# Kernel tuning notes

Hardware: AMD Instinct MI355X
Metric: run time of the kernel (lower is better)

The kernel has to match this reference:

```python
import jax, jax.numpy as jnp
import numpy as np

SMALL = 1e-16
N = 8192      # num_nodes
D_IN = 512    # input_dim
D_LAT = 128   # latent_dim


def setup_inputs() -> dict:
    key = jax.random.key(0)
    ks = jax.random.split(key, 6)
    z = jax.random.normal(ks[0], (N, D_IN), jnp.float32)
    gamma = jax.random.uniform(ks[1], (N, D_IN), jnp.float32)
    delta = jax.random.uniform(ks[2], (N, D_IN), jnp.float32)
    lim = float(np.sqrt(6.0 / (D_IN + D_LAT)))  # glorot-uniform init
    Wz = jax.random.uniform(ks[3], (D_IN, D_LAT), jnp.float32, -lim, lim)
    Wg = jax.random.uniform(ks[4], (D_IN, D_LAT), jnp.float32, -lim, lim)
    Wd = jax.random.uniform(ks[5], (D_IN, D_LAT), jnp.float32, -lim, lim)
    return {
        "z": z, "gamma": gamma, "delta": delta,
        "Wz": Wz, "Wg": Wg, "Wd": Wd,
        "bias": jnp.float32(1.0),
        "w_gam": jnp.float32(0.5),
        "w_del": jnp.float32(0.5),
    }


def reference(z, gamma, delta, Wz, Wg, Wd, bias, w_gam, w_del):
    # column-stochastic transforms (softmax over input_dim axis, as in __init__)
    Tz = jax.nn.softmax(Wz, axis=0)
    Tg = jax.nn.softmax(Wg, axis=0)
    Td = jax.nn.softmax(Wd, axis=0)

    zd = z @ Tz                 # [N, D_LAT]
    gd_raw = gamma @ Tg         # [N, D_LAT]
    dd_raw = delta @ Td         # [N, D_LAT]
    gd = gd_raw + SMALL
    dd = dd_raw + SMALL

    z2 = zd * zd
    # dist_gam[i,j] = sum_k (zd[i,k]-zd[j,k])^2 / gd[i,k]  (sender-scaled)
    # expanded: sum_k z2_i/g_i  +  (1/g_i) . z2_j  -  2 (z_i/g_i) . z_j
    a = jnp.sum(z2 / gd, axis=1)                                  # [N]
    dist_gam = a[:, None] + (1.0 / gd) @ z2.T - 2.0 * (zd / gd) @ zd.T  # [N,N]

    # dist_del[i,j] = sum_k (zd[i,k]-zd[j,k])^2 / dd[j,k]  (receiver-scaled)
    b = jnp.sum(z2 / dd, axis=1)                                  # [N]
    dist_del = z2 @ (1.0 / dd).T - 2.0 * zd @ (zd / dd).T + b[None, :]  # [N,N]

    n = jnp.float32(N)
    x = bias - w_gam * (n * dist_gam) - w_del * (n * dist_del)
    out = jax.nn.sigmoid(x.reshape(-1))                           # [N*N]
    return out, zd, gd_raw, dd_raw
```

## Files before the change

### kernel.cpp

```cpp
#include <hip/hip_runtime.h>
#include <hip/hip_bf16.h>
#include <math.h>


#define NSZ 8192
#define DLAT 128

typedef _Float16 half8 __attribute__((ext_vector_type(8)));
typedef float f32x4 __attribute__((ext_vector_type(4)));
typedef float f32x16 __attribute__((ext_vector_type(16)));

__device__ __forceinline__ void gl_lds16(const void* g, void* l) {
    __builtin_amdgcn_global_load_lds(
        (const __attribute__((address_space(1))) void*)g,
        (__attribute__((address_space(3))) void*)l, 16, 0, 0);
}

__device__ __forceinline__ float fast_sigmoid(float x) {
    float e = __builtin_amdgcn_exp2f(-1.44269504f * x);
    return __builtin_amdgcn_rcpf(1.0f + e);
}

__global__ void softmax_cols(const float* __restrict__ Wz, const float* __restrict__ Wg,
                             const float* __restrict__ Wd, _Float16* __restrict__ Tt) {
    int col = blockIdx.x & 127;
    int m = blockIdx.x >> 7;
    const float* W = (m == 0) ? Wz : (m == 1 ? Wg : Wd);
    _Float16* To = Tt + (size_t)m * 65536 + (size_t)col * 512;
    int l = threadIdx.x;
    float v[8];
    float mx = -3.4e38f;
    for (int i = 0; i < 8; ++i) {
        v[i] = W[(size_t)(i * 64 + l) * 128 + col];
        mx = fmaxf(mx, v[i]);
    }
    for (int off = 32; off; off >>= 1) mx = fmaxf(mx, __shfl_xor(mx, off));
    float s = 0.f;
    for (int i = 0; i < 8; ++i) { v[i] = expf(v[i] - mx); s += v[i]; }
    for (int off = 32; off; off >>= 1) s += __shfl_xor(s, off);
    float inv = 1.0f / s;
    for (int i = 0; i < 8; ++i) To[i * 64 + l] = (_Float16)(v[i] * inv);
}

__global__ __launch_bounds__(128) void gemm3_mfma(const float* __restrict__ z,
                                                  const float* __restrict__ gamma,
                                                  const float* __restrict__ delta,
                                                  const _Float16* __restrict__ Tt,
                                                  float* __restrict__ outTail) {
    int m = blockIdx.y;
    const float* A = (m == 0) ? z : (m == 1 ? gamma : delta);
    const _Float16* B = Tt + (size_t)m * 65536;
    float* C = outTail + (size_t)m * (NSZ * DLAT);
    int rowBase = blockIdx.x * 32;
    __shared__ _Float16 As[32 * 520];
    int t = threadIdx.x;
    for (int s = 0; s < 16; ++s) {
        int id = s * 128 + t;
        int row = id >> 6, c8 = id & 63;
        const float4* src = (const float4*)(A + (size_t)(rowBase + row) * 512 + c8 * 8);
        float4 f0 = src[0], f1 = src[1];
        half8 h = {(_Float16)f0.x, (_Float16)f0.y, (_Float16)f0.z, (_Float16)f0.w,
                   (_Float16)f1.x, (_Float16)f1.y, (_Float16)f1.z, (_Float16)f1.w};
        *(half8*)(&As[row * 520 + c8 * 8]) = h;
    }
    __syncthreads();

    int l = t & 63, w = t >> 6;
    int lc = l & 15, lq = l >> 4;
    int m0 = w * 16;
    f32x4 acc[8] = {};
    for (int kt = 0; kt < 16; ++kt) {
        int k0 = kt * 32;
        half8 af = *(const half8*)(&As[(m0 + lc) * 520 + k0 + lq * 8]);
        for (int ni = 0; ni < 8; ++ni) {
            half8 bf = *(const half8*)(B + (size_t)(ni * 16 + lc) * 512 + k0 + lq * 8);
            acc[ni] = __builtin_amdgcn_mfma_f32_16x16x32_f16(af, bf, acc[ni], 0, 0, 0);
        }
    }
    for (int ni = 0; ni < 8; ++ni) {
        for (int r = 0; r < 4; ++r) {
            int row = rowBase + m0 + lq * 4 + r;
            int col = ni * 16 + lc;
            C[(size_t)row * 128 + col] = acc[ni][r];
        }
    }
}

__global__ void build_stacks(const float* __restrict__ zd, const float* __restrict__ gdr,
                             const float* __restrict__ ddr, _Float16* __restrict__ Afp,
                             _Float16* __restrict__ Bfp, float* __restrict__ cvec,
                             float* __restrict__ bco, const float* __restrict__ pb,
                             const float* __restrict__ pwg, const float* __restrict__ pwd) {
    int i = blockIdx.x;
    int k = threadIdx.x;
    float zv = zd[(size_t)i * 128 + k];
    float g = gdr[(size_t)i * 128 + k] + 1e-16f;
    float d = ddr[(size_t)i * 128 + k] + 1e-16f;
    float z2 = zv * zv;
    float u = 1.0f / g, p = 1.0f / d;
    float wg = *pwg, wd = *pwd, bias = *pb;
    _Float16* Ar = Afp + (size_t)i * 512;
    _Float16* Br = Bfp + (size_t)i * 512;
    Ar[k]       = (_Float16)(wg * u);
    Ar[128 + k] = (_Float16)(wg * zv * u);
    Ar[256 + k] = (_Float16)(wd * z2);
    Ar[384 + k] = (_Float16)(wd * zv);
    Br[k]       = (_Float16)(z2);
    Br[128 + k] = (_Float16)(-2.0f * zv);
    Br[256 + k] = (_Float16)(p);
    Br[384 + k] = (_Float16)(-2.0f * zv * p);
    float a = z2 * u, b = z2 * p;
    for (int off = 32; off; off >>= 1) { a += __shfl_down(a, off); b += __shfl_down(b, off); }
    __shared__ float sa[2], sb[2];
    if ((k & 63) == 0) { sa[k >> 6] = a; sb[k >> 6] = b; }
    __syncthreads();
    if (k == 0) {
        cvec[i] = bias - 8192.0f * wg * (sa[0] + sa[1]);
        bco[i] = 8192.0f * wd * (sb[0] + sb[1]);
    }
}

__global__ __launch_bounds__(256) void pair_kernel(const _Float16* __restrict__ Afp,
                                                   const _Float16* __restrict__ Bfp,
                                                   const float* __restrict__ cvec,
                                                   const float* __restrict__ bco,
                                                   const float* __restrict__ pbias,
                                                   float* __restrict__ out) {
    int bid = blockIdx.x;
    int super = bid >> 6, within = bid & 63;
    int sy = super >> 3, sx = super & 7;
    int by = sy * 8 + (within >> 3), bx = sx * 8 + (within & 7);
    int iBase = by * 128, jBase = bx * 128;

    __shared__ _Float16 As[128 * 64];
    __shared__ _Float16 Bs[128 * 64];
    int t = threadIdx.x;
    int l = t & 63, w = t >> 6;
    int wm = (w >> 1) * 64, wn = (w & 1) * 64;
    int ln = l & 31, lh = l >> 5;
    f32x16 acc[2][2] = {};

    int srow = l >> 3;
    int sq = (l & 7) ^ srow;

    for (int kt = 0; kt < 8; ++kt) {
        int k0 = kt * 64;
        for (int s = 0; s < 4; ++s) {
            int rr = (w * 4 + s) * 8 + srow;
            const _Float16* ga = Afp + (size_t)(iBase + rr) * 512 + k0 + sq * 8;
            const _Float16* gb = Bfp + (size_t)(jBase + rr) * 512 + k0 + sq * 8;
            gl_lds16(ga, &As[(w * 4 + s) * 512]);
            gl_lds16(gb, &Bs[(w * 4 + s) * 512]);
        }
        __syncthreads();
        for (int ks = 0; ks < 4; ++ks) {
            int q = ks * 2 + lh;
            half8 af[2], bf[2];
            for (int m2 = 0; m2 < 2; ++m2) {
                int r = wm + m2 * 32 + ln;
                af[m2] = *(const half8*)(&As[((r << 3) + (q ^ (r & 7))) << 3]);
            }
            for (int n2 = 0; n2 < 2; ++n2) {
                int r = wn + n2 * 32 + ln;
                bf[n2] = *(const half8*)(&Bs[((r << 3) + (q ^ (r & 7))) << 3]);
            }
            for (int m2 = 0; m2 < 2; ++m2)
                for (int n2 = 0; n2 < 2; ++n2)
                    acc[m2][n2] = __builtin_amdgcn_mfma_f32_32x32x16_f16(af[m2], bf[n2],
                                                                         acc[m2][n2], 0, 0, 0);
        }
        __syncthreads();
    }

    float bias = *pbias;
    bool diagBlock = (iBase == jBase);
    float bjv[2];
    for (int n2 = 0; n2 < 2; ++n2) bjv[n2] = bco[jBase + wn + n2 * 32 + ln];

    for (int m2 = 0; m2 < 2; ++m2) {
        float civ[16];
        for (int reg = 0; reg < 16; ++reg)
            civ[reg] = cvec[iBase + wm + m2 * 32 + (reg & 3) + 8 * (reg >> 2) + 4 * lh];
        for (int n2 = 0; n2 < 2; ++n2) {
            int j = jBase + wn + n2 * 32 + ln;
            for (int reg = 0; reg < 16; ++reg) {
                int i = iBase + wm + m2 * 32 + (reg & 3) + 8 * (reg >> 2) + 4 * lh;
                float x = civ[reg] - bjv[n2] - 8192.0f * acc[m2][n2][reg];
                if (diagBlock) { if (i == j) x = bias; }
                out[(size_t)i * NSZ + j] = fast_sigmoid(x);
            }
        }
    }
}

extern "C" void kernel_launch(void* const* d_in, const int* in_sizes, int n_in,
                              void* d_out, int out_size, void* d_ws, size_t ws_size,
                              hipStream_t stream) {
    const float* z = (const float*)d_in[0];
    const float* gamma = (const float*)d_in[1];
    const float* delta = (const float*)d_in[2];
    const float* Wz = (const float*)d_in[3];
    const float* Wg = (const float*)d_in[4];
    const float* Wd = (const float*)d_in[5];
    const float* pb = (const float*)d_in[6];
    const float* pwg = (const float*)d_in[7];
    const float* pwd = (const float*)d_in[8];

    float* out = (float*)d_out;
    float* zd_out = out + (size_t)NSZ * NSZ;
    float* gd_out = zd_out + (size_t)NSZ * DLAT;
    float* dd_out = gd_out + (size_t)NSZ * DLAT;

    float* wsf = (float*)d_ws;
    _Float16* Tt = (_Float16*)wsf;
    float* cvec = wsf + 98304;
    float* bco = cvec + 8192;
    _Float16* Afp = (_Float16*)(bco + 8192);
    _Float16* Bfp = Afp + (size_t)NSZ * 512;

    softmax_cols<<<384, 64, 0, stream>>>(Wz, Wg, Wd, Tt);
    gemm3_mfma<<<dim3(256, 3), 128, 0, stream>>>(z, gamma, delta, Tt, zd_out);
    build_stacks<<<NSZ, 128, 0, stream>>>(zd_out, gd_out, dd_out, Afp, Bfp, cvec, bco,
                                          pb, pwg, pwd);
    pair_kernel<<<4096, 256, 0, stream>>>(Afp, Bfp, cvec, bco, pb, out);
}
```

Baseline: 414.0 us.

## Double-buffer LDS tiles in pair kernel and hoist epilogue vector loads

The pair kernel now keeps two LDS stages for the A and B tiles. It prefetches the next K slice with global_load_lds while MFMAs run on the current slice, which drops one of the two barriers per iteration. The cvec and bco loads move ahead of the main loop so their latency overlaps the GEMM, and launch bounds request 2 blocks per CU. The cost is twice the LDS per block and extra registers held live through the loop, which may limit occupancy. The kernel looks dominated by output stores, so the overlap may matter little.

```diff
diff --git a/kernel.cpp b/kernel.cpp
--- a/kernel.cpp
+++ b/kernel.cpp
@@ -120,20 +120,20 @@
     }
 }
 
-__global__ __launch_bounds__(256) void pair_kernel(const _Float16* __restrict__ Afp,
-                                                   const _Float16* __restrict__ Bfp,
-                                                   const float* __restrict__ cvec,
-                                                   const float* __restrict__ bco,
-                                                   const float* __restrict__ pbias,
-                                                   float* __restrict__ out) {
+__global__ __launch_bounds__(256, 2) void pair_kernel(const _Float16* __restrict__ Afp,
+                                                      const _Float16* __restrict__ Bfp,
+                                                      const float* __restrict__ cvec,
+                                                      const float* __restrict__ bco,
+                                                      const float* __restrict__ pbias,
+                                                      float* __restrict__ out) {
     int bid = blockIdx.x;
     int super = bid >> 6, within = bid & 63;
     int sy = super >> 3, sx = super & 7;
     int by = sy * 8 + (within >> 3), bx = sx * 8 + (within & 7);
     int iBase = by * 128, jBase = bx * 128;
 
-    __shared__ _Float16 As[128 * 64];
-    __shared__ _Float16 Bs[128 * 64];
+    __shared__ _Float16 As[2][128 * 64];
+    __shared__ _Float16 Bs[2][128 * 64];
     int t = threadIdx.x;
     int l = t & 63, w = t >> 6;
     int wm = (w >> 1) * 64, wn = (w & 1) * 64;
@@ -142,50 +142,59 @@
 
     int srow = l >> 3;
     int sq = (l & 7) ^ srow;
+    const _Float16* gA0 = Afp + (size_t)iBase * 512 + sq * 8;
+    const _Float16* gB0 = Bfp + (size_t)jBase * 512 + sq * 8;
+
+    float bias = *pbias;
+    float bjv[2];
+    for (int n2 = 0; n2 < 2; ++n2) bjv[n2] = bco[jBase + wn + n2 * 32 + ln];
+    float civ[2][16];
+    for (int m2 = 0; m2 < 2; ++m2)
+        for (int reg = 0; reg < 16; ++reg)
+            civ[m2][reg] = cvec[iBase + wm + m2 * 32 + (reg & 3) + 8 * (reg >> 2) + 4 * lh];
+
+    for (int s = 0; s < 4; ++s) {
+        int rr = (w * 4 + s) * 8 + srow;
+        gl_lds16(gA0 + (size_t)rr * 512, &As[0][(w * 4 + s) * 512]);
+        gl_lds16(gB0 + (size_t)rr * 512, &Bs[0][(w * 4 + s) * 512]);
+    }
 
     for (int kt = 0; kt < 8; ++kt) {
-        int k0 = kt * 64;
-        for (int s = 0; s < 4; ++s) {
-            int rr = (w * 4 + s) * 8 + srow;
-            const _Float16* ga = Afp + (size_t)(iBase + rr) * 512 + k0 + sq * 8;
-            const _Float16* gb = Bfp + (size_t)(jBase + rr) * 512 + k0 + sq * 8;
-            gl_lds16(ga, &As[(w * 4 + s) * 512]);
-            gl_lds16(gb, &Bs[(w * 4 + s) * 512]);
-        }
+        int cur = kt & 1;
         __syncthreads();
+        if (kt < 7) {
+            int k1 = (kt + 1) * 64;
+            for (int s = 0; s < 4; ++s) {
+                int rr = (w * 4 + s) * 8 + srow;
+                gl_lds16(gA0 + (size_t)rr * 512 + k1, &As[cur ^ 1][(w * 4 + s) * 512]);
+                gl_lds16(gB0 + (size_t)rr * 512 + k1, &Bs[cur ^ 1][(w * 4 + s) * 512]);
+            }
+        }
         for (int ks = 0; ks < 4; ++ks) {
             int q = ks * 2 + lh;
             half8 af[2], bf[2];
             for (int m2 = 0; m2 < 2; ++m2) {
                 int r = wm + m2 * 32 + ln;
-                af[m2] = *(const half8*)(&As[((r << 3) + (q ^ (r & 7))) << 3]);
+                af[m2] = *(const half8*)(&As[cur][((r << 3) + (q ^ (r & 7))) << 3]);
             }
             for (int n2 = 0; n2 < 2; ++n2) {
                 int r = wn + n2 * 32 + ln;
-                bf[n2] = *(const half8*)(&Bs[((r << 3) + (q ^ (r & 7))) << 3]);
+                bf[n2] = *(const half8*)(&Bs[cur][((r << 3) + (q ^ (r & 7))) << 3]);
             }
             for (int m2 = 0; m2 < 2; ++m2)
                 for (int n2 = 0; n2 < 2; ++n2)
                     acc[m2][n2] = __builtin_amdgcn_mfma_f32_32x32x16_f16(af[m2], bf[n2],
                                                                          acc[m2][n2], 0, 0, 0);
         }
-        __syncthreads();
-    }
-
-    float bias = *pbias;
+    }
+
     bool diagBlock = (iBase == jBase);
-    float bjv[2];
-    for (int n2 = 0; n2 < 2; ++n2) bjv[n2] = bco[jBase + wn + n2 * 32 + ln];
-
     for (int m2 = 0; m2 < 2; ++m2) {
-        float civ[16];
-        for (int reg = 0; reg < 16; ++reg)
-            civ[reg] = cvec[iBase + wm + m2 * 32 + (reg & 3) + 8 * (reg >> 2) + 4 * lh];
         for (int n2 = 0; n2 < 2; ++n2) {
             int j = jBase + wn + n2 * 32 + ln;
             for (int reg = 0; reg < 16; ++reg) {
                 int i = iBase + wm + m2 * 32 + (reg & 3) + 8 * (reg >> 2) + 4 * lh;
-                float x = civ[reg] - bjv[n2] - 8192.0f * acc[m2][n2][reg];
+                float x = civ[m2][reg] - bjv[n2] - 8192.0f * acc[m2][n2][reg];
                 if (diagBlock) { if (i == j) x = bias; }
                 out[(size_t)i * NSZ + j] = fast_sigmoid(x);
             }
```

After: 432.9 us. 4.6% more time.
